# Performance work log

Hardware: AMD Instinct MI355X
Metric: run time of the kernel (lower is better)

The kernel has to match this reference:

```python
import jax, jax.numpy as jnp
import numpy as np

SEQ_LEN, INPUT_DIM, HIDDEN_DIM, NUM_CLASSES, BATCH = 512, 256, 1024, 128, 256


def setup_inputs() -> dict:
    key = jax.random.key(0)
    ks = jax.random.split(key, 12)
    sx = np.sqrt(2.0 / INPUT_DIM).astype(np.float32)
    sh = np.sqrt(2.0 / HIDDEN_DIM).astype(np.float32)
    inp = {
        "x": jax.random.randint(ks[0], (BATCH, SEQ_LEN, 1), 0, NUM_CLASSES, dtype=jnp.int32),
        "emb": jax.random.normal(ks[1], (NUM_CLASSES, INPUT_DIM), jnp.float32),
        "Wcx": jax.random.normal(ks[2], (HIDDEN_DIM, INPUT_DIM), jnp.float32) * sx,
        "bc": jnp.zeros((HIDDEN_DIM,), jnp.float32),
        "Wix": jax.random.normal(ks[3], (HIDDEN_DIM, INPUT_DIM), jnp.float32) * sx,
        "Wih": jax.random.normal(ks[4], (HIDDEN_DIM, HIDDEN_DIM), jnp.float32) * sh,
        "bi": jnp.zeros((HIDDEN_DIM,), jnp.float32),
        "Wfx": jax.random.normal(ks[5], (HIDDEN_DIM, INPUT_DIM), jnp.float32) * sx,
        "Wfh": jax.random.normal(ks[6], (HIDDEN_DIM, HIDDEN_DIM), jnp.float32) * sh,
        "bf": jnp.zeros((HIDDEN_DIM,), jnp.float32),
        "Wox": jax.random.normal(ks[7], (HIDDEN_DIM, INPUT_DIM), jnp.float32) * sx,
        "Woh": jax.random.normal(ks[8], (HIDDEN_DIM, HIDDEN_DIM), jnp.float32) * sh,
        "bo": jnp.zeros((HIDDEN_DIM,), jnp.float32),
        "Wph": jax.random.normal(ks[9], (NUM_CLASSES, HIDDEN_DIM), jnp.float32) * sh,
        "bp": jnp.zeros((NUM_CLASSES,), jnp.float32),
    }
    return inp


def reference(x, emb, Wcx, bc, Wix, Wih, bi, Wfx, Wfh, bf, Wox, Woh, bo, Wph, bp):
    B = x.shape[0]
    H = Wfh.shape[0]
    xt = emb[x[:, :, 0]]                       # [B, S, I] embedded inputs
    # Precompute the input-to-gate projections (parallel over time; identical math)
    xf = jnp.einsum("bsi,hi->sbh", xt, Wfx)    # [S, B, H]
    xi = jnp.einsum("bsi,hi->sbh", xt, Wix)
    xo = jnp.einsum("bsi,hi->sbh", xt, Wox)
    xc = jnp.einsum("bsi,hi->sbh", xt, Wcx)

    def step(carry, inputs):
        c, h = carry
        xf_t, xi_t, xo_t, xc_t = inputs
        # peephole gates read cell state c, not h
        f = jax.nn.sigmoid(xf_t + c @ Wfh.T + bf)
        i = jax.nn.sigmoid(xi_t + c @ Wih.T + bi)
        o = jax.nn.sigmoid(xo_t + c @ Woh.T + bo)
        c_new = jax.nn.sigmoid(xc_t + bc) * i + c * f
        h_new = jnp.tanh(c_new) * o
        return (c_new, h_new), None

    c0 = jnp.zeros((B, H), xt.dtype)
    h0 = jnp.zeros((B, H), xt.dtype)
    (c_T, h_T), _ = jax.lax.scan(step, (c0, h0), (xf, xi, xo, xc))
    p = h_T @ Wph.T + bp                       # [B, num_classes]
    return jax.nn.log_softmax(p, axis=1)
```

## Files before the change

kernel.cpp:

```cpp
#include <hip/hip_runtime.h>

#define SEQ  512
#define IDIM 256
#define H    1024
#define NC   128
#define B    256
#define NBLK 256

typedef __attribute__((ext_vector_type(8))) short bh8;
typedef __attribute__((ext_vector_type(4))) float f4;
typedef __attribute__((ext_vector_type(4))) int i4;

__device__ __forceinline__ float sigf(float x) { return 1.0f / (1.0f + __expf(-x)); }

__device__ __forceinline__ unsigned short bf16r(float v) {
    unsigned u = __builtin_bit_cast(unsigned, v);
    u += 0x7fffu + ((u >> 16) & 1u);
    return (unsigned short)(u >> 16);
}

__global__ __launch_bounds__(256) void tables_kernel(
    const float* __restrict__ emb,
    const float* __restrict__ Wcx, const float* __restrict__ bc,
    const float* __restrict__ Wix, const float* __restrict__ bi,
    const float* __restrict__ Wfx, const float* __restrict__ bf,
    const float* __restrict__ Wox, const float* __restrict__ bo,
    float* __restrict__ FF, float* __restrict__ II,
    float* __restrict__ OO, float* __restrict__ G)
{
    const int k = blockIdx.x;
    const int h = blockIdx.y * 256 + threadIdx.x;
    __shared__ float e[IDIM];
    e[threadIdx.x] = emb[k * IDIM + threadIdx.x];
    __syncthreads();
    const float4* e4  = (const float4*)e;
    const float4* wf4 = (const float4*)(Wfx + (size_t)h * IDIM);
    const float4* wi4 = (const float4*)(Wix + (size_t)h * IDIM);
    const float4* wo4 = (const float4*)(Wox + (size_t)h * IDIM);
    const float4* wc4 = (const float4*)(Wcx + (size_t)h * IDIM);
    float aF = 0.f, aI = 0.f, aO = 0.f, aC = 0.f;
#pragma unroll 4
    for (int i = 0; i < IDIM / 4; i++) {
        float4 ev = e4[i];
        float4 a = wf4[i]; aF += ev.x * a.x + ev.y * a.y + ev.z * a.z + ev.w * a.w;
        float4 b = wi4[i]; aI += ev.x * b.x + ev.y * b.y + ev.z * b.z + ev.w * b.w;
        float4 c = wo4[i]; aO += ev.x * c.x + ev.y * c.y + ev.z * c.z + ev.w * c.w;
        float4 d = wc4[i]; aC += ev.x * d.x + ev.y * d.y + ev.z * d.z + ev.w * d.w;
    }
    const int o = k * H + h;
    FF[o] = aF + bf[h];
    II[o] = aI + bi[h];
    OO[o] = aO + bo[h];
    G[o]  = sigf(aC + bc[h]);
}

__global__ __launch_bounds__(256) void swz_kernel(const float* __restrict__ W,
                                                  unsigned short* __restrict__ D)
{
    int g = blockIdx.x * 256 + threadIdx.x;
    int h  = g >> 7;
    int kc = (g & 127) << 3;
    const float4* s = (const float4*)(W + (size_t)h * H + kc);
    float4 a = s[0], b = s[1];
    unsigned short tmp[8] = { bf16r(a.x), bf16r(a.y), bf16r(a.z), bf16r(a.w),
                              bf16r(b.x), bf16r(b.y), bf16r(b.z), bf16r(b.w) };
    int nb = h >> 4, kb = kc >> 5, quad = (kc >> 3) & 3;
    int lane = (h & 15) + (quad << 4);
    bh8 v;
#pragma unroll
    for (int j = 0; j < 8; j++) v[j] = (short)tmp[j];
    *(bh8*)(D + (size_t)((nb * 32 + kb) * 512 + lane * 8)) = v;
}

__global__ __launch_bounds__(256, 1) void persist_kernel(
    const unsigned short* __restrict__ Wf, const unsigned short* __restrict__ Wi,
    const unsigned short* __restrict__ Wo,
    const float* __restrict__ FF, const float* __restrict__ II,
    const float* __restrict__ OO, const float* __restrict__ G,
    const int* __restrict__ x,
    unsigned short* c16a, unsigned short* c16b,
    float* __restrict__ hb, int* flags)
{
    const int blk = blockIdx.x;
    const int rt = blk >> 4;
    const int nt = blk & 15;
    const int tid  = threadIdx.x;
    const int wave = tid >> 6;
    const int lane = tid & 63;
    const int l15 = lane & 15, quad = lane >> 4;

    __shared__ unsigned short cs[16 * 1024];

    const int row0 = rt * 16;
    const int abase = l15 * 1024;
    const int asw = l15 & 7;
    const int hcol = nt * 64 + wave * 16 + l15;
    const int nb = nt * 4 + wave;

    const unsigned short* wfp = Wf + (size_t)nb * 32 * 512 + (size_t)lane * 8;
    const unsigned short* wip = Wi + (size_t)nb * 32 * 512 + (size_t)lane * 8;
    const unsigned short* wop = Wo + (size_t)nb * 32 * 512 + (size_t)lane * 8;

    bh8 wf_r[32], wi_r[32];
#pragma unroll
    for (int kt = 0; kt < 32; kt++) {
        wf_r[kt] = *(const bh8*)(wfp + (size_t)kt * 512);
        wi_r[kt] = *(const bh8*)(wip + (size_t)kt * 512);
    }

    float cn_keep[4] = {0.f, 0.f, 0.f, 0.f};
    int* const myflag = flags + blk;
    const int* const pf = flags + rt * 16 + l15;

    for (int s = 0; s < SEQ; s++) {
        const unsigned short* cur16 = (s & 1) ? c16b : c16a;
        unsigned short*       nxt16 = (s & 1) ? c16a : c16b;

        float ffv[4], iiv[4], ggv[4];
#pragma unroll
        for (int r = 0; r < 4; r++) {
            int b = row0 + quad * 4 + r;
            int tok = x[b * SEQ + s];
            ffv[r] = FF[tok * H + hcol];
            iiv[r] = II[tok * H + hcol];
            ggv[r] = G[tok * H + hcol];
        }

        f4 accF = {0.f, 0.f, 0.f, 0.f}, accI = {0.f, 0.f, 0.f, 0.f};
        if (s > 0) {
            i4 tmp[8];
#pragma unroll
            for (int i = 0; i < 8; i++) {
                int chunk = i * 256 + tid;
                int row = chunk >> 7, g = chunk & 127;
                const i4* p = (const i4*)(cur16 + (size_t)(row0 + row) * H + g * 8);
                asm volatile("global_load_dwordx4 %0, %1, off sc0 sc1"
                             : "=v"(tmp[i]) : "v"(p));
            }
            asm volatile("s_waitcnt vmcnt(0)" ::: "memory");
#pragma unroll
            for (int i = 0; i < 8; i++) {
                int chunk = i * 256 + tid;
                int row = chunk >> 7, g = chunk & 127;
                *(i4*)(cs + row * 1024 + ((g ^ (row & 7)) << 3)) = tmp[i];
            }
            __syncthreads();
#pragma unroll
            for (int kt = 0; kt < 32; kt++) {
                bh8 a = *(const bh8*)(cs + abase + (((kt * 4 + quad) ^ asw) << 3));
                accF = __builtin_amdgcn_mfma_f32_16x16x32_bf16(a, wf_r[kt], accF, 0, 0, 0);
                accI = __builtin_amdgcn_mfma_f32_16x16x32_bf16(a, wi_r[kt], accI, 0, 0, 0);
            }
        }

#pragma unroll
        for (int r = 0; r < 4; r++) {
            float f = sigf(ffv[r] + accF[r]);
            float i = sigf(iiv[r] + accI[r]);
            float cn = ggv[r] * i + cn_keep[r] * f;
            cn_keep[r] = cn;
            int b = row0 + quad * 4 + r;
            unsigned us = bf16r(cn);
            unsigned ot = (unsigned)__shfl_xor((int)us, 1);
            if (s < SEQ - 1 && (lane & 1) == 0)
                __hip_atomic_store((unsigned*)(nxt16 + (size_t)b * H + hcol), us | (ot << 16),
                                   __ATOMIC_RELAXED, __HIP_MEMORY_SCOPE_AGENT);
        }

        if (s < SEQ - 1) {
            __syncthreads();
            if (wave == 0) {
                if (lane == 0) {
                    int v = s + 1;
                    asm volatile("global_store_dword %0, %1, off sc0 sc1"
                                 :: "v"(myflag), "v"(v) : "memory");
                }
                const int target = s + 1;
                int guard = 0;
                for (;;) {
                    int fv;
                    asm volatile("global_load_dword %0, %1, off sc0 sc1\n\ts_waitcnt vmcnt(0)"
                                 : "=v"(fv) : "v"(pf) : "memory");
                    if (__all(fv >= target)) break;
                    if (++guard > (1 << 20)) break;
                }
            }
            __syncthreads();
        }
    }

    f4 accO = {0.f, 0.f, 0.f, 0.f};
#pragma unroll 4
    for (int kt = 0; kt < 32; kt++) {
        bh8 a  = *(const bh8*)(cs + abase + (((kt * 4 + quad) ^ asw) << 3));
        bh8 bo = *(const bh8*)(wop + (size_t)kt * 512);
        accO = __builtin_amdgcn_mfma_f32_16x16x32_bf16(a, bo, accO, 0, 0, 0);
    }
#pragma unroll
    for (int r = 0; r < 4; r++) {
        int b = row0 + quad * 4 + r;
        int tok = x[b * SEQ + (SEQ - 1)];
        float o = sigf(OO[tok * H + hcol] + accO[r]);
        hb[(size_t)b * H + hcol] = tanhf(cn_keep[r]) * o;
    }
}

__global__ __launch_bounds__(128) void out_kernel(
    const float* __restrict__ hbuf, const float* __restrict__ Wph,
    const float* __restrict__ bp, float* __restrict__ out)
{
    const int b = blockIdx.x;
    const int j = threadIdx.x;
    __shared__ float hs[H];
    for (int t = j; t < H; t += 128) hs[t] = hbuf[(size_t)b * H + t];
    __syncthreads();
    const float4* w4 = (const float4*)(Wph + (size_t)j * H);
    const float4* h4 = (const float4*)hs;
    float acc = bp[j];
#pragma unroll 4
    for (int k = 0; k < H / 4; k++) {
        float4 a = w4[k], v = h4[k];
        acc += a.x * v.x + a.y * v.y + a.z * v.z + a.w * v.w;
    }
    __shared__ float red[128];
    red[j] = acc; __syncthreads();
    for (int off = 64; off > 0; off >>= 1) { if (j < off) red[j] = fmaxf(red[j], red[j + off]); __syncthreads(); }
    float m = red[0]; __syncthreads();
    red[j] = __expf(acc - m); __syncthreads();
    for (int off = 64; off > 0; off >>= 1) { if (j < off) red[j] += red[j + off]; __syncthreads(); }
    float lse = m + __logf(red[0]);
    out[(size_t)b * NC + j] = acc - lse;
}

extern "C" void kernel_launch(void* const* d_in, const int* in_sizes, int n_in,
                              void* d_out, int out_size, void* d_ws, size_t ws_size,
                              hipStream_t stream)
{
    const int*   x   = (const int*)d_in[0];
    const float* emb = (const float*)d_in[1];
    const float* Wcx = (const float*)d_in[2];
    const float* bc  = (const float*)d_in[3];
    const float* Wix = (const float*)d_in[4];
    const float* Wih = (const float*)d_in[5];
    const float* bi  = (const float*)d_in[6];
    const float* Wfx = (const float*)d_in[7];
    const float* Wfh = (const float*)d_in[8];
    const float* bf  = (const float*)d_in[9];
    const float* Wox = (const float*)d_in[10];
    const float* Woh = (const float*)d_in[11];
    const float* bo  = (const float*)d_in[12];
    const float* Wph = (const float*)d_in[13];
    const float* bp  = (const float*)d_in[14];
    float* out = (float*)d_out;

    char* wsb = (char*)d_ws;
    float* FF = (float*)(wsb + 0);
    float* II = (float*)(wsb + (512 << 10));
    float* OO = (float*)(wsb + (1024 << 10));
    float* G  = (float*)(wsb + (1536 << 10));
    float* hb = (float*)(wsb + (2048 << 10));
    int*   flags = (int*)(wsb + (3072 << 10));
    unsigned short* Wf_sw = (unsigned short*)(wsb + (4096 << 10));
    unsigned short* Wi_sw = (unsigned short*)(wsb + (6144 << 10));
    unsigned short* Wo_sw = (unsigned short*)(wsb + (8192 << 10));
    unsigned short* c16a  = (unsigned short*)(wsb + (10240 << 10));
    unsigned short* c16b  = (unsigned short*)(wsb + (10752 << 10));

    hipMemsetAsync(flags, 0, 1024, stream);

    tables_kernel<<<dim3(NC, 4), 256, 0, stream>>>(emb, Wcx, bc, Wix, bi, Wfx, bf, Wox, bo,
                                                   FF, II, OO, G);
    swz_kernel<<<512, 256, 0, stream>>>(Wfh, Wf_sw);
    swz_kernel<<<512, 256, 0, stream>>>(Wih, Wi_sw);
    swz_kernel<<<512, 256, 0, stream>>>(Woh, Wo_sw);

    persist_kernel<<<NBLK, 256, 0, stream>>>(Wf_sw, Wi_sw, Wo_sw, FF, II, OO, G, x,
                                             c16a, c16b, hb, flags);

    out_kernel<<<B, 128, 0, stream>>>(hb, Wph, bp, out);
}
```

Baseline: 2.699 ms.

## Replace flag barrier with step-tagged data exchange between persistent blocks

Each exchanged cell-state word now carries its bf16 value in the high half and the timestep tag in the low half. Consumers poll the data words directly until every tag matches the current step. This removes the separate per-block flag store, the spin-wait on flags and two __syncthreads per step, so producer-to-consumer latency shrinks. In exchange the exchange buffer doubles in bytes and is read with 64-bit atomic loads. Tags left in the workspace from a previous launch could match the current step, which may let a stale value be accepted.

```diff
diff --git a/kernel.cpp b/kernel.cpp
--- a/kernel.cpp
+++ b/kernel.cpp
@@ -9,7 +9,7 @@
 
 typedef __attribute__((ext_vector_type(8))) short bh8;
 typedef __attribute__((ext_vector_type(4))) float f4;
-typedef __attribute__((ext_vector_type(4))) int i4;
+typedef unsigned long long u64;
 
 __device__ __forceinline__ float sigf(float x) { return 1.0f / (1.0f + __expf(-x)); }
 
@@ -78,15 +78,15 @@
     const float* __restrict__ FF, const float* __restrict__ II,
     const float* __restrict__ OO, const float* __restrict__ G,
     const int* __restrict__ x,
-    unsigned short* c16a, unsigned short* c16b,
-    float* __restrict__ hb, int* flags)
+    unsigned* exa, unsigned* exb,
+    float* __restrict__ hb)
 {
     const int blk = blockIdx.x;
     const int rt = blk >> 4;
     const int nt = blk & 15;
     const int tid  = threadIdx.x;
+    const int lane = tid & 63;
     const int wave = tid >> 6;
-    const int lane = tid & 63;
     const int l15 = lane & 15, quad = lane >> 4;
 
     __shared__ unsigned short cs[16 * 1024];
@@ -109,12 +109,10 @@
     }
 
     float cn_keep[4] = {0.f, 0.f, 0.f, 0.f};
-    int* const myflag = flags + blk;
-    const int* const pf = flags + rt * 16 + l15;
 
     for (int s = 0; s < SEQ; s++) {
-        const unsigned short* cur16 = (s & 1) ? c16b : c16a;
-        unsigned short*       nxt16 = (s & 1) ? c16a : c16b;
+        const unsigned* excur = (s & 1) ? exb : exa;
+        unsigned*       exnxt = (s & 1) ? exa : exb;
 
         float ffv[4], iiv[4], ggv[4];
 #pragma unroll
@@ -128,28 +126,51 @@
 
         f4 accF = {0.f, 0.f, 0.f, 0.f}, accI = {0.f, 0.f, 0.f, 0.f};
         if (s > 0) {
-            i4 tmp[8];
-#pragma unroll
-            for (int i = 0; i < 8; i++) {
-                int chunk = i * 256 + tid;
-                int row = chunk >> 7, g = chunk & 127;
-                const i4* p = (const i4*)(cur16 + (size_t)(row0 + row) * H + g * 8);
-                asm volatile("global_load_dwordx4 %0, %1, off sc0 sc1"
-                             : "=v"(tmp[i]) : "v"(p));
-            }
-            asm volatile("s_waitcnt vmcnt(0)" ::: "memory");
-#pragma unroll
-            for (int i = 0; i < 8; i++) {
-                int chunk = i * 256 + tid;
-                int row = chunk >> 7, g = chunk & 127;
-                *(i4*)(cs + row * 1024 + ((g ^ (row & 7)) << 3)) = tmp[i];
+            u64 a[16], bwd[16];
+            const unsigned* exrow = excur + (size_t)row0 * H + tid * 4;
+#pragma unroll
+            for (int i = 0; i < 16; i++) {
+                const u64* p = (const u64*)(exrow + i * H);
+                a[i]   = __hip_atomic_load(p,     __ATOMIC_RELAXED, __HIP_MEMORY_SCOPE_AGENT);
+                bwd[i] = __hip_atomic_load(p + 1, __ATOMIC_RELAXED, __HIP_MEMORY_SCOPE_AGENT);
+            }
+            unsigned fresh = 0;
+            int guard = 0;
+            const u64 t0 = (unsigned)s;
+            for (;;) {
+#pragma unroll
+                for (int i = 0; i < 16; i++) {
+                    if (!(fresh & (1u << i))) {
+                        bool ok = ((a[i] & 0xffffu) == t0) && (((a[i] >> 32) & 0xffffu) == t0) &&
+                                  ((bwd[i] & 0xffffu) == t0) && (((bwd[i] >> 32) & 0xffffu) == t0);
+                        if (ok) fresh |= (1u << i);
+                    }
+                }
+                if (__all(fresh == 0xffffu)) break;
+                if (++guard > (1 << 17)) break;
+#pragma unroll
+                for (int i = 0; i < 16; i++) {
+                    if (!(fresh & (1u << i))) {
+                        const u64* p = (const u64*)(exrow + i * H);
+                        a[i]   = __hip_atomic_load(p,     __ATOMIC_RELAXED, __HIP_MEMORY_SCOPE_AGENT);
+                        bwd[i] = __hip_atomic_load(p + 1, __ATOMIC_RELAXED, __HIP_MEMORY_SCOPE_AGENT);
+                    }
+                }
+            }
+            const int g = tid >> 1, half = tid & 1;
+#pragma unroll
+            for (int i = 0; i < 16; i++) {
+                unsigned p0 = (unsigned)(((a[i] >> 16) & 0xffffu)   | ((a[i] >> 32) & 0xffff0000u));
+                unsigned p1 = (unsigned)(((bwd[i] >> 16) & 0xffffu) | ((bwd[i] >> 32) & 0xffff0000u));
+                u64 v = ((u64)p1 << 32) | p0;
+                *(u64*)(cs + i * 1024 + ((g ^ (i & 7)) << 3) + (half << 2)) = v;
             }
             __syncthreads();
 #pragma unroll
             for (int kt = 0; kt < 32; kt++) {
-                bh8 a = *(const bh8*)(cs + abase + (((kt * 4 + quad) ^ asw) << 3));
-                accF = __builtin_amdgcn_mfma_f32_16x16x32_bf16(a, wf_r[kt], accF, 0, 0, 0);
-                accI = __builtin_amdgcn_mfma_f32_16x16x32_bf16(a, wi_r[kt], accI, 0, 0, 0);
+                bh8 av = *(const bh8*)(cs + abase + (((kt * 4 + quad) ^ asw) << 3));
+                accF = __builtin_amdgcn_mfma_f32_16x16x32_bf16(av, wf_r[kt], accF, 0, 0, 0);
+                accI = __builtin_amdgcn_mfma_f32_16x16x32_bf16(av, wi_r[kt], accI, 0, 0, 0);
             }
         }
 
@@ -160,41 +181,20 @@
             float cn = ggv[r] * i + cn_keep[r] * f;
             cn_keep[r] = cn;
             int b = row0 + quad * 4 + r;
-            unsigned us = bf16r(cn);
-            unsigned ot = (unsigned)__shfl_xor((int)us, 1);
-            if (s < SEQ - 1 && (lane & 1) == 0)
-                __hip_atomic_store((unsigned*)(nxt16 + (size_t)b * H + hcol), us | (ot << 16),
+            if (s < SEQ - 1) {
+                unsigned d = ((unsigned)bf16r(cn) << 16) | (unsigned)(s + 1);
+                __hip_atomic_store(exnxt + (size_t)b * H + hcol, d,
                                    __ATOMIC_RELAXED, __HIP_MEMORY_SCOPE_AGENT);
-        }
-
-        if (s < SEQ - 1) {
-            __syncthreads();
-            if (wave == 0) {
-                if (lane == 0) {
-                    int v = s + 1;
-                    asm volatile("global_store_dword %0, %1, off sc0 sc1"
-                                 :: "v"(myflag), "v"(v) : "memory");
-                }
-                const int target = s + 1;
-                int guard = 0;
-                for (;;) {
-                    int fv;
-                    asm volatile("global_load_dword %0, %1, off sc0 sc1\n\ts_waitcnt vmcnt(0)"
-                                 : "=v"(fv) : "v"(pf) : "memory");
-                    if (__all(fv >= target)) break;
-                    if (++guard > (1 << 20)) break;
-                }
-            }
-            __syncthreads();
+            }
         }
     }
 
     f4 accO = {0.f, 0.f, 0.f, 0.f};
 #pragma unroll 4
     for (int kt = 0; kt < 32; kt++) {
-        bh8 a  = *(const bh8*)(cs + abase + (((kt * 4 + quad) ^ asw) << 3));
+        bh8 av = *(const bh8*)(cs + abase + (((kt * 4 + quad) ^ asw) << 3));
         bh8 bo = *(const bh8*)(wop + (size_t)kt * 512);
-        accO = __builtin_amdgcn_mfma_f32_16x16x32_bf16(a, bo, accO, 0, 0, 0);
+        accO = __builtin_amdgcn_mfma_f32_16x16x32_bf16(av, bo, accO, 0, 0, 0);
     }
 #pragma unroll
     for (int r = 0; r < 4; r++) {
@@ -259,14 +259,11 @@
     float* OO = (float*)(wsb + (1024 << 10));
     float* G  = (float*)(wsb + (1536 << 10));
     float* hb = (float*)(wsb + (2048 << 10));
-    int*   flags = (int*)(wsb + (3072 << 10));
     unsigned short* Wf_sw = (unsigned short*)(wsb + (4096 << 10));
     unsigned short* Wi_sw = (unsigned short*)(wsb + (6144 << 10));
     unsigned short* Wo_sw = (unsigned short*)(wsb + (8192 << 10));
-    unsigned short* c16a  = (unsigned short*)(wsb + (10240 << 10));
-    unsigned short* c16b  = (unsigned short*)(wsb + (10752 << 10));
-
-    hipMemsetAsync(flags, 0, 1024, stream);
+    unsigned* exa = (unsigned*)(wsb + (10240 << 10));
+    unsigned* exb = (unsigned*)(wsb + (11264 << 10));
 
     tables_kernel<<<dim3(NC, 4), 256, 0, stream>>>(emb, Wcx, bc, Wix, bi, Wfx, bf, Wox, bo,
                                                    FF, II, OO, G);
@@ -275,7 +272,7 @@
     swz_kernel<<<512, 256, 0, stream>>>(Woh, Wo_sw);
 
     persist_kernel<<<NBLK, 256, 0, stream>>>(Wf_sw, Wi_sw, Wo_sw, FF, II, OO, G, x,
-                                             c16a, c16b, hb, flags);
+                                             exa, exb, hb);
 
     out_kernel<<<B, 128, 0, stream>>>(hb, Wph, bp, out);
 }
```

After: 3.774 ms. +39.8%, slower.
